# Kernel tuning notes

Hardware: AMD Instinct MI355X
Metric: run time of the kernel (lower is better)

Reference implementation:

```python
import jax, jax.numpy as jnp
import numpy as np

B = 4
NV = 6890           # SMPL vertex count
NF0 = 13776         # SMPL face count (before fill_back)
T = 3               # tex_size
IMG = 128           # render image size
UVH = UVW = 256     # uv image resolution
FLENGTH = 500.0
NEAR, FAR = 0.1, 25.0
CHUNK = 128         # faces per z-buffer scan step
BIG = jnp.float32(1e10)


def setup_inputs():
    key = jax.random.key(0)
    ks = jax.random.split(key, 5)
    faces0 = jax.random.randint(ks[0], (NF0, 3), 0, NV, dtype=jnp.int32)
    faces = jnp.concatenate([faces0, faces0[:, ::-1]], axis=0)  # fill_back
    cam = jnp.concatenate([0.8 + 0.2 * jax.random.uniform(ks[1], (B, 1)),
                           0.05 * jax.random.normal(ks[2], (B, 2))], axis=1)
    vertices = 0.3 * jax.random.normal(ks[3], (B, NV, 3))
    uv_imgs = jax.random.uniform(ks[4], (B, 3, UVH, UVW))
    img2uv_sampler = jax.random.uniform(jax.random.fold_in(key, 7),
                                        (faces.shape[0], T * T, 2)) * 2.0 - 1.0
    return {"cam": cam, "vertices": vertices, "uv_imgs": uv_imgs,
            "img2uv_sampler": img2uv_sampler, "faces": faces}


def _grid_sample(img, grid):
    # img (B,C,H,W), grid (B,N,2) xy in [-1,1]; bilinear, align_corners=False, zeros padding
    Bc, C, H, W = img.shape
    x = (grid[..., 0] + 1.0) * (W * 0.5) - 0.5
    y = (grid[..., 1] + 1.0) * (H * 0.5) - 0.5
    x0f = jnp.floor(x); y0f = jnp.floor(y)
    wx = x - x0f; wy = y - y0f
    x0 = x0f.astype(jnp.int32); y0 = y0f.astype(jnp.int32)
    imgf = img.reshape(Bc, C, H * W)
    def gat(yi, xi, w):
        valid = (xi >= 0) & (xi < W) & (yi >= 0) & (yi < H)
        idx = jnp.clip(yi, 0, H - 1) * W + jnp.clip(xi, 0, W - 1)
        v = jax.vmap(lambda im, i: im[:, i])(imgf, idx)  # (B,C,N)
        return v * (w * valid)[:, None, :]
    return (gat(y0, x0, (1 - wx) * (1 - wy)) + gat(y0, x0 + 1, wx * (1 - wy)) +
            gat(y0 + 1, x0, (1 - wx) * wy) + gat(y0 + 1, x0 + 1, wx * wy))


def _extract_tex(uv_imgs, sampler, nf):
    # sampler (B,nf,T*T,2) -> textures (B,nf,T,T,T,3)
    tex = _grid_sample(uv_imgs, sampler.reshape(uv_imgs.shape[0], -1, 2))
    tex = tex.reshape(-1, 3, nf, T, T).transpose(0, 2, 3, 4, 1)  # (B,nf,T,T,3)
    return jnp.broadcast_to(tex[:, :, :, :, None, :], tex.shape[:4] + (T, 3))


def _lighting(face_verts, textures):
    # module defaults: ambient intensity 1, directional 0, white lights, dir=(0,1,0)
    v0, v1, v2 = face_verts[:, :, 0], face_verts[:, :, 1], face_verts[:, :, 2]
    n = jnp.cross(v1 - v0, v2 - v0)
    n = n / (jnp.linalg.norm(n, axis=-1, keepdims=True) + 1e-10)
    cos = jnp.maximum(n @ jnp.array([0.0, 1.0, 0.0]), 0.0)       # (B,F)
    light = 1.0 * jnp.ones(3) + 0.0 * cos[..., None] * jnp.ones(3)  # (B,F,3)
    return textures * light[:, :, None, None, None, :]


def _weak_projection(cam, vertices):
    p = IMG / 2.0
    tz = FLENGTH / (p * cam[:, 0:1])                              # (B,1)
    v2d = cam[:, None, 0:1] * (vertices[:, :, :2] + cam[:, None, 1:])
    return jnp.concatenate([v2d, vertices[:, :, 2:3] + tz[:, None, :]], axis=-1)


def _bary(fv, px, py):
    # fv: (...,3,3) triangle screen verts; px,py broadcastable pixel coords
    x0 = fv[..., 0, 0]; y0 = fv[..., 0, 1]
    x1 = fv[..., 1, 0]; y1 = fv[..., 1, 1]
    x2 = fv[..., 2, 0]; y2 = fv[..., 2, 1]
    w0 = (x2 - x1) * (py - y1) - (y2 - y1) * (px - x1)
    w1 = (x0 - x2) * (py - y2) - (y0 - y2) * (px - x2)
    w2 = (x1 - x0) * (py - y0) - (y1 - y0) * (px - x0)
    area = w0 + w1 + w2
    s = jnp.where(area == 0, 1.0, area)
    return w0 / s, w1 / s, w2 / s, area


def _pixel_grid():
    xs = (2.0 * jnp.arange(IMG) + 1.0) / IMG - 1.0                # (W,)
    ys = (1.0 - (2.0 * jnp.arange(IMG) + 1.0) / IMG)[:, None]     # (H,1), +y up
    return xs, ys


def _rasterize_fim(face_verts):
    # face_verts (B,F,3,3) in screen coords -> face index map (B,H,W), -1 = bg
    Bc, F = face_verts.shape[:2]
    pad = (-F) % CHUNK
    fv = jnp.pad(face_verts, ((0, 0), (0, pad), (0, 0), (0, 0)))
    S = (F + pad) // CHUNK
    fv = fv.reshape(Bc, S, CHUNK, 3, 3).transpose(1, 0, 2, 3, 4)  # (S,B,C,3,3)
    xs, ys = _pixel_grid()
    def step(carry, inp):
        zbuf, fim = carry
        f, base = inp
        fe = f[:, :, None, None, :, :]                            # (B,C,1,1,3,3)
        b0, b1, b2, area = _bary(fe, xs, ys)                      # (B,C,H,W)
        z0 = f[:, :, 0, 2][..., None, None]
        z1 = f[:, :, 1, 2][..., None, None]
        z2 = f[:, :, 2, 2][..., None, None]
        invz = b0 / z0 + b1 / z1 + b2 / z2                        # perspective-correct
        zp = 1.0 / jnp.where(invz == 0, 1.0, invz)
        inside = (b0 >= 0) & (b1 >= 0) & (b2 >= 0) & (area > 0)   # front-facing only
        valid = inside & (zp > NEAR) & (zp < FAR)
        depth = jnp.where(valid, zp, BIG)
        dmin = jnp.min(depth, axis=1)                             # (B,H,W)
        amin = jnp.argmin(depth, axis=1).astype(jnp.int32) + base
        better = dmin < zbuf
        return (jnp.where(better, dmin, zbuf),
                jnp.where(better, amin, fim)), None
    zbuf0 = jnp.full((Bc, IMG, IMG), BIG)
    fim0 = jnp.full((Bc, IMG, IMG), -1, jnp.int32)
    bases = (jnp.arange(S) * CHUNK).astype(jnp.int32)
    (zbuf, fim), _ = jax.lax.scan(step, (zbuf0, fim0), (fv, bases))
    return fim


def _shade(face_verts, textures, fim):
    # nearest-texel barycentric texture lookup, as in neural_renderer forward
    Bc, F = face_verts.shape[:2]
    fid = jnp.clip(fim, 0, F - 1).reshape(Bc, -1)                 # (B,HW)
    fv = jax.vmap(lambda v, i: v[i])(face_verts, fid)             # (B,HW,3,3)
    fv = fv.reshape(Bc, IMG, IMG, 3, 3)
    xs, ys = _pixel_grid()
    b0, b1, b2, _ = _bary(fv, xs, ys)                             # (B,H,W)
    t0 = jnp.clip(jnp.floor(b0 * T).astype(jnp.int32), 0, T - 1)
    t1 = jnp.clip(jnp.floor(b1 * T).astype(jnp.int32), 0, T - 1)
    t2 = jnp.clip(jnp.floor(b2 * T).astype(jnp.int32), 0, T - 1)
    idx = ((jnp.clip(fim, 0, F - 1) * T + t0) * T + t1) * T + t2  # (B,H,W)
    texf = textures.reshape(Bc, F * T * T * T, 3)
    col = jax.vmap(lambda t, i: t[i])(texf, idx.reshape(Bc, -1))  # (B,HW,3)
    col = col.reshape(Bc, IMG, IMG, 3)
    col = jnp.where((fim >= 0)[..., None], col, 0.0)              # bg color (0,0,0)
    return col.transpose(0, 3, 1, 2)                              # (B,3,H,W)


def reference(cam, vertices, uv_imgs, img2uv_sampler, faces):
    Bc = cam.shape[0]
    nf = faces.shape[0]
    sampler = jnp.broadcast_to(img2uv_sampler[None], (Bc,) + img2uv_sampler.shape)
    textures = _extract_tex(uv_imgs, sampler, nf)                 # (B,nf,T,T,T,3)
    textures = _lighting(vertices[:, faces], textures)
    verts_p = _weak_projection(cam, vertices)
    fv = verts_p[:, faces]                                        # (B,nf,3,3)
    fv_sg = jax.lax.stop_gradient(fv)  # hard rasterization is non-differentiable
    fim = _rasterize_fim(fv_sg)
    images = _shade(fv_sg, textures, fim)
    return images


if __name__ == "__main__":
    out = reference(**setup_inputs())
    print(out.shape, out.dtype)
```

## Files before the change

### kernel.cpp

```cpp
#include <hip/hip_runtime.h>
#include <stdint.h>

#pragma clang fp contract(off)

#define B_    4
#define NV_   6890
#define NF_   27552
#define IMG_  128
#define UV_   256
#define NPIX  (IMG_*IMG_)

#define TS_     8
#define TPB_    (IMG_/TS_)
#define NTILE_  (TPB_*TPB_)
#define NBIN_   (B_*NTILE_)
#define LIST_CAP (2*1024*1024)
#define MAXC_   (LIST_CAP/256 + NBIN_)

__global__ void __launch_bounds__(256) project_k(
    const float* __restrict__ cam, const float* __restrict__ verts,
    float* __restrict__ vp) {
  int idx = blockIdx.x * 256 + threadIdx.x;
  if (idx >= B_ * NV_) return;
  int b = idx / NV_;
  float c0 = cam[b * 3 + 0], c1 = cam[b * 3 + 1], c2 = cam[b * 3 + 2];
  float tz = 500.0f / (64.0f * c0);
  const float* src = verts + (size_t)idx * 3;
  float* dst = vp + (size_t)idx * 3;
  dst[0] = c0 * (src[0] + c1);
  dst[1] = c0 * (src[1] + c2);
  dst[2] = src[2] + tz;
}

__device__ __forceinline__ int face_tiles(
    const float* __restrict__ vp, const int* __restrict__ faces, int b, int f,
    int& tx0, int& tx1, int& ty0, int& ty1, unsigned& z16) {
  int ia = faces[f * 3 + 0], ib = faces[f * 3 + 1], ic = faces[f * 3 + 2];
  const float* vb = vp + (size_t)b * NV_ * 3;
  float x0 = vb[ia * 3 + 0], y0 = vb[ia * 3 + 1];
  float x1 = vb[ib * 3 + 0], y1 = vb[ib * 3 + 1];
  float x2 = vb[ic * 3 + 0], y2 = vb[ic * 3 + 1];
  float area_c = (x1 - x0) * (y2 - y0) - (y1 - y0) * (x2 - x0);
  if (area_c < -1e-3f) return 0;
  float xmn = fminf(x0, fminf(x1, x2)), xmx = fmaxf(x0, fmaxf(x1, x2));
  float ymn = fminf(y0, fminf(y1, y2)), ymx = fmaxf(y0, fmaxf(y1, y2));
  int jlo = (int)floorf((xmn + 1.0f) * 64.0f - 0.5f) - 1;
  int jhi = (int)ceilf ((xmx + 1.0f) * 64.0f - 0.5f) + 1;
  int ilo = (int)floorf((1.0f - ymx) * 64.0f - 0.5f) - 1;
  int ihi = (int)ceilf ((1.0f - ymn) * 64.0f - 0.5f) + 1;
  if (jhi < 0 || ihi < 0 || jlo > IMG_ - 1 || ilo > IMG_ - 1) return 0;
  jlo = max(jlo, 0); ilo = max(ilo, 0);
  jhi = min(jhi, IMG_ - 1); ihi = min(ihi, IMG_ - 1);
  tx0 = jlo >> 3; tx1 = jhi >> 3; ty0 = ilo >> 3; ty1 = ihi >> 3;
  float z0 = vb[ia * 3 + 2], z1 = vb[ib * 3 + 2], z2 = vb[ic * 3 + 2];
  z16 = __float_as_uint(fminf(z0, fminf(z1, z2))) >> 16;
  return 1;
}

__global__ void __launch_bounds__(256) bin_count_k(
    const float* __restrict__ vp, const int* __restrict__ faces,
    int* __restrict__ cnt, int* __restrict__ rects) {
  __shared__ int scnt[NTILE_];
  int f = blockIdx.x * 256 + threadIdx.x;
  int b = blockIdx.y;
  scnt[threadIdx.x] = 0;
  __syncthreads();
  int tx0, tx1, ty0, ty1;
  unsigned z16 = 0;
  int valid =
      (f < NF_) ? face_tiles(vp, faces, b, f, tx0, tx1, ty0, ty1, z16) : 0;
  if (f < NF_)
    rects[(size_t)b * NF_ + f] =
        valid ? (int)((z16 << 16) | (unsigned)(tx0 | (tx1 << 4) | (ty0 << 8) |
                                               (ty1 << 12)))
              : (int)0xFFFF0000u;
  if (valid)
    for (int ty = ty0; ty <= ty1; ++ty)
      for (int tx = tx0; tx <= tx1; ++tx)
        atomicAdd(&scnt[ty * TPB_ + tx], 1);
  __syncthreads();
  int t = threadIdx.x;
  int v = scnt[t];
  if (v > 0) atomicAdd(&cnt[b * NTILE_ + t], v);
}

__global__ void __launch_bounds__(1024) scan_k(
    const int* __restrict__ cnt, int* __restrict__ off, int* __restrict__ cur,
    int* __restrict__ work, int* __restrict__ nC) {
  __shared__ int sm[NBIN_];
  int t = threadIdx.x;
  int v = cnt[t];
  sm[t] = v;
  __syncthreads();
  for (int d = 1; d < NBIN_; d <<= 1) {
    int u = (t >= d) ? sm[t - d] : 0;
    __syncthreads();
    sm[t] += u;
    __syncthreads();
  }
  int o = sm[t] - v;
  off[t] = o;
  cur[t] = o;
  int nch = (max(v - 256, 0) + 255) >> 8;
  __syncthreads();
  sm[t] = nch;
  __syncthreads();
  for (int d = 1; d < NBIN_; d <<= 1) {
    int u = (t >= d) ? sm[t - d] : 0;
    __syncthreads();
    sm[t] += u;
    __syncthreads();
  }
  int cb = sm[t] - nch;
  if (t == NBIN_ - 1) nC[0] = sm[t];
  for (int c = 0; c < nch; ++c) work[cb + c] = t | ((c + 1) << 10);
}

__global__ void __launch_bounds__(256) bin_fill_k(
    const int* __restrict__ rects, int* __restrict__ cur,
    int* __restrict__ list) {
  __shared__ int scnt[NTILE_];
  __shared__ int sbase[NTILE_];
  int f = blockIdx.x * 256 + threadIdx.x;
  int b = blockIdx.y;
  scnt[threadIdx.x] = 0;
  __syncthreads();
  unsigned rv =
      (f < NF_) ? (unsigned)rects[(size_t)b * NF_ + f] : 0xFFFF0000u;
  unsigned hi = rv >> 16;
  int valid = (hi != 0xFFFFu);
  int tx0 = rv & 15, tx1 = (rv >> 4) & 15;
  int ty0 = (rv >> 8) & 15, ty1 = (rv >> 12) & 15;
  if (valid)
    for (int ty = ty0; ty <= ty1; ++ty)
      for (int tx = tx0; tx <= tx1; ++tx)
        atomicAdd(&scnt[ty * TPB_ + tx], 1);
  __syncthreads();
  int t = threadIdx.x;
  int v = scnt[t];
  if (v > 0) sbase[t] = atomicAdd(&cur[b * NTILE_ + t], v);
  __syncthreads();
  scnt[t] = 0;
  __syncthreads();
  if (valid) {
    int ev = (int)((hi << 15) | (unsigned)f);
    for (int ty = ty0; ty <= ty1; ++ty)
      for (int tx = tx0; tx <= tx1; ++tx) {
        int bin = ty * TPB_ + tx;
        int r = atomicAdd(&scnt[bin], 1);
        int slot = sbase[bin] + r;
        if (slot < LIST_CAP) list[slot] = ev;
      }
  }
}

__device__ __forceinline__ void raster_slice(
    const float4 (*F)[64], int nsurv, float px, float py,
    unsigned long long& kb, unsigned& kbz_u) {
  unsigned win_u = 0x7F800000u;
  unsigned long long qm = 0ull;
  for (int q = 0; q < nsurv; ++q) {
    float4 A = F[0][q];
    float4 Bv = F[1][q];
    float4 Cv = F[2][q];
    float w0 = A.x * (py - A.w) - A.y * (px - A.z);
    float w1 = Bv.x * (py - Bv.w) - Bv.y * (px - Bv.z);
    float w2 = Cv.x * (py - Cv.w) - Cv.y * (px - Cv.z);
    float area = (w0 + w1) + w2;
    float mn = fminf(w0, fminf(w1, w2));
    bool pred = (area > 0.0f) && !(mn < 0.0f);
    if (!__any(pred)) continue;
    float4 P = F[4][q];
    float num = (w0 * P.x + w1 * P.y) + w2 * P.z;
    float zpa = (area * P.w) * __builtin_amdgcn_rcpf(num);
    unsigned cu = win_u < kbz_u ? win_u : kbz_u;
    float thrq = __uint_as_float(cu) * 1.001f;
    bool amb = pred && (!(zpa > thrq) ||
                        (zpa > 0.09989f && zpa < 0.10011f) ||
                        (zpa > 24.9724f && zpa < 25.0276f));
    if (amb) qm |= 1ull << q;
    bool ok = pred && (zpa > 0.1001f) && (zpa < 24.975f);
    unsigned zb = __float_as_uint(zpa);
    if (ok && zb < win_u) win_u = zb;
  }
  while (__any(qm != 0ull)) {
    if (qm != 0ull) {
      int q = __ffsll(qm) - 1;
      qm &= qm - 1ull;
      float4 A = F[0][q];
      float4 Bv = F[1][q];
      float4 Cv = F[2][q];
      float w0 = A.x * (py - A.w) - A.y * (px - A.z);
      float w1 = Bv.x * (py - Bv.w) - Bv.y * (px - Bv.z);
      float w2 = Cv.x * (py - Cv.w) - Cv.y * (px - Cv.z);
      float area = (w0 + w1) + w2;
      float4 P = F[4][q];
      float num = (w0 * P.x + w1 * P.y) + w2 * P.z;
      float zpa = (area * P.w) * __builtin_amdgcn_rcpf(num);
      unsigned cu = win_u < kbz_u ? win_u : kbz_u;
      float thrf = __uint_as_float(cu) * 1.001f;
      if (!(zpa > thrf) ||
          (zpa > 0.09989f && zpa < 0.10011f) ||
          (zpa > 24.9724f && zpa < 25.0276f)) {
        float4 Z = F[3][q];
        float b0 = w0 / area, b1 = w1 / area, b2 = w2 / area;
        float invz = (b0 / Z.x + b1 / Z.y) + b2 / Z.z;
        float zp = 1.0f / (invz == 0.0f ? 1.0f : invz);
        if (zp > 0.1f && zp < 25.0f) {
          unsigned long long key =
              ((unsigned long long)__float_as_uint(zp) << 32) |
              (unsigned int)__float_as_int(Z.w);
          if (key < kb) {
            kb = key;
            kbz_u = (unsigned)(kb >> 32);
          }
        }
      }
    }
  }
}

__device__ __forceinline__ void stage_face(
    float4 (*F)[64], const float* __restrict__ vb,
    const int* __restrict__ faces, int fid, int rank) {
  int ia = faces[fid * 3 + 0], ib = faces[fid * 3 + 1], ic = faces[fid * 3 + 2];
  float X0 = vb[ia * 3 + 0], Y0 = vb[ia * 3 + 1], Z0 = vb[ia * 3 + 2];
  float X1 = vb[ib * 3 + 0], Y1 = vb[ib * 3 + 1], Z1 = vb[ib * 3 + 2];
  float X2 = vb[ic * 3 + 0], Y2 = vb[ic * 3 + 1], Z2 = vb[ic * 3 + 2];
  F[0][rank] = make_float4(X2 - X1, Y2 - Y1, X1, Y1);
  F[1][rank] = make_float4(X0 - X2, Y0 - Y2, X2, Y2);
  F[2][rank] = make_float4(X1 - X0, Y1 - Y0, X0, Y0);
  F[3][rank] = make_float4(Z0, Z1, Z2, __int_as_float(fid));
  F[4][rank] = make_float4(Z1 * Z2, Z0 * Z2, Z0 * Z1, Z0 * Z1 * Z2);
}

__global__ void __launch_bounds__(256) raster_seed_k(
    const float* __restrict__ vp, const int* __restrict__ faces,
    const int* __restrict__ list, const int* __restrict__ cnt,
    const int* __restrict__ off, unsigned long long* __restrict__ zkey) {
  __shared__ float4 fd[4][5][64];
  __shared__ unsigned long long mg[4][64];
  int bin = blockIdx.x;
  int b = bin >> 8;
  int t = bin & 255;
  int tyT = t >> 4, txT = t & 15;
  int ws = threadIdx.x >> 6, lane = threadIdx.x & 63;
  int pi = tyT * TS_ + (lane >> 3);
  int pj = txT * TS_ + (lane & 7);
  float px = fmaf((float)pj, 0.015625f, -0.9921875f);
  float py = fmaf((float)pi, -0.015625f, 0.9921875f);

  int n = min(cnt[bin], 256);
  int base = off[bin];
  int seg = ws * 64;
  int mw = min(n - seg, 64);

  unsigned long long kb = ~0ull;
  unsigned kbz_u = 0x7F800000u;
  if (mw > 0) {
    if (lane < mw) {
      int fid = (int)((unsigned)list[base + seg + lane] & 0x7FFFu);
      stage_face(fd[ws], vp + (size_t)b * NV_ * 3, faces, fid, lane);
    }
    raster_slice(fd[ws], mw, px, py, kb, kbz_u);
  }

  mg[ws][lane] = kb;
  __syncthreads();
  if (ws == 0) {
    unsigned long long k0 = mg[0][lane];
    unsigned long long k1 = mg[1][lane];
    unsigned long long k2 = mg[2][lane];
    unsigned long long k3 = mg[3][lane];
    k0 = k1 < k0 ? k1 : k0;
    k2 = k3 < k2 ? k3 : k2;
    k0 = k2 < k0 ? k2 : k0;
    zkey[(size_t)b * NPIX + pi * IMG_ + pj] = k0;
  }
}

__global__ void __launch_bounds__(256) raster_k(
    const float* __restrict__ vp, const int* __restrict__ faces,
    const int* __restrict__ list, const int* __restrict__ cnt,
    const int* __restrict__ off, const int* __restrict__ work,
    const int* __restrict__ nC, unsigned long long* __restrict__ zkey) {
  __shared__ float4 fd[4][5][64];
  __shared__ unsigned long long mg[4][64];
  __shared__ unsigned sdz[64];
  int bid = blockIdx.x;
  if (bid >= nC[0]) return;
  int wkv = work[bid];
  int bin = wkv & (NBIN_ - 1);
  int chunk = wkv >> 10;
  int b = bin >> 8;
  int t = bin & 255;
  int tyT = t >> 4, txT = t & 15;
  int ws = threadIdx.x >> 6, lane = threadIdx.x & 63;
  int pi = tyT * TS_ + (lane >> 3);
  int pj = txT * TS_ + (lane & 7);
  float px = fmaf((float)pj, 0.015625f, -0.9921875f);
  float py = fmaf((float)pi, -0.015625f, 0.9921875f);

  if (threadIdx.x < 64) {
    unsigned long long s = atomicMin(
        zkey + (size_t)b * NPIX + (tyT * TS_ + (threadIdx.x >> 3)) * IMG_ +
            txT * TS_ + (threadIdx.x & 7),
        ~0ull);
    sdz[threadIdx.x] = (unsigned)(s >> 32);
  }
  __syncthreads();

  unsigned seed_u = min(sdz[lane], 0x7F800000u);
  unsigned mx = seed_u;
  for (int j = 1; j < 64; j <<= 1) {
    unsigned o = (unsigned)__shfl_xor((int)mx, j, 64);
    mx = o > mx ? o : mx;
  }
  unsigned thr_code = __float_as_uint(__uint_as_float(mx) * 1.01f) >> 16;

  int n = cnt[bin];
  int seg = (chunk << 8) + (ws << 6);
  int base0 = off[bin] + seg;
  int mw = min(n - seg, 64);
  mw = max(mw, 0);

  bool live = false;
  int fid = 0;
  if (lane < mw) {
    unsigned e = (unsigned)list[base0 + lane];
    live = ((e >> 15) <= thr_code);
    fid = (int)(e & 0x7FFFu);
  }
  unsigned long long bal = __ballot(live);
  unsigned long long kb = ~0ull;
  unsigned kbz_u = seed_u;
  if (bal != 0ull) {
    int nsurv = (int)__popcll(bal);
    int rank = (int)__popcll(bal & ((1ull << lane) - 1ull));
    if (live)
      stage_face(fd[ws], vp + (size_t)b * NV_ * 3, faces, fid, rank);
    raster_slice(fd[ws], nsurv, px, py, kb, kbz_u);
  }

  mg[ws][lane] = kb;
  __syncthreads();
  if (ws == 0) {
    unsigned long long k0 = mg[0][lane];
    unsigned long long k1 = mg[1][lane];
    unsigned long long k2 = mg[2][lane];
    unsigned long long k3 = mg[3][lane];
    k0 = k1 < k0 ? k1 : k0;
    k2 = k3 < k2 ? k3 : k2;
    k0 = k2 < k0 ? k2 : k0;
    if (k0 != ~0ull)
      atomicMin(zkey + (size_t)b * NPIX + pi * IMG_ + pj, k0);
  }
}

#define TAP(ty, tx, wexpr)                                                   \
  {                                                                          \
    int ty_ = (ty), tx_ = (tx);                                              \
    float w_ = (wexpr);                                                      \
    float valid_ =                                                           \
        (tx_ >= 0 && tx_ < UV_ && ty_ >= 0 && ty_ < UV_) ? 1.0f : 0.0f;      \
    float wv_ = w_ * valid_;                                                 \
    int cy_ = min(max(ty_, 0), UV_ - 1), cx_ = min(max(tx_, 0), UV_ - 1);    \
    int o_ = cy_ * UV_ + cx_;                                                \
    cr = cr + img[o_] * wv_;                                                 \
    cg = cg + img[UV_ * UV_ + o_] * wv_;                                     \
    cb = cb + img[2 * UV_ * UV_ + o_] * wv_;                                 \
  }

__global__ void __launch_bounds__(256) shade_k(
    const float* __restrict__ vp, const int* __restrict__ faces,
    const float* __restrict__ uv, const float* __restrict__ samp,
    const unsigned long long* __restrict__ zkey, float* __restrict__ out) {
  int idx = blockIdx.x * 256 + threadIdx.x;
  if (idx >= B_ * NPIX) return;
  int b = idx / NPIX;
  int p = idx - b * NPIX;
  int ii = p / IMG_;
  int jj = p - ii * IMG_;

  unsigned long long key = zkey[idx];
  float cr = 0.0f, cg = 0.0f, cb = 0.0f;
  if (key != 0xFFFFFFFFFFFFFFFFull) {
    int f = (int)(key & 0xFFFFFFFFull);
    int ia = faces[f * 3 + 0], ib = faces[f * 3 + 1], ic = faces[f * 3 + 2];
    const float* vb = vp + (size_t)b * NV_ * 3;
    float x0 = vb[ia * 3 + 0], y0 = vb[ia * 3 + 1];
    float x1 = vb[ib * 3 + 0], y1 = vb[ib * 3 + 1];
    float x2 = vb[ic * 3 + 0], y2 = vb[ic * 3 + 1];
    float px = (float)(2 * jj + 1) / 128.0f - 1.0f;
    float py = 1.0f - (float)(2 * ii + 1) / 128.0f;
    float w0 = (x2 - x1) * (py - y1) - (y2 - y1) * (px - x1);
    float w1 = (x0 - x2) * (py - y2) - (y0 - y2) * (px - x2);
    float w2 = (x1 - x0) * (py - y0) - (y1 - y0) * (px - x0);
    float area = (w0 + w1) + w2;
    float s = (area == 0.0f) ? 1.0f : area;
    float b0 = w0 / s, b1 = w1 / s;
    int t0 = min(max((int)floorf(b0 * 3.0f), 0), 2);
    int t1 = min(max((int)floorf(b1 * 3.0f), 0), 2);

    const float* g = samp + ((size_t)f * 9 + (size_t)(t0 * 3 + t1)) * 2;
    float gx = g[0], gy = g[1];
    float x = (gx + 1.0f) * 128.0f - 0.5f;
    float y = (gy + 1.0f) * 128.0f - 0.5f;
    float x0f = floorf(x), y0f = floorf(y);
    float wx = x - x0f, wy = y - y0f;
    int xi = (int)x0f, yi = (int)y0f;
    float omwx = 1.0f - wx, omwy = 1.0f - wy;
    const float* img = uv + (size_t)b * 3 * UV_ * UV_;
    TAP(yi,     xi,     omwx * omwy)
    TAP(yi,     xi + 1, wx * omwy)
    TAP(yi + 1, xi,     omwx * wy)
    TAP(yi + 1, xi + 1, wx * wy)
  }
  out[((size_t)b * 3 + 0) * NPIX + p] = cr;
  out[((size_t)b * 3 + 1) * NPIX + p] = cg;
  out[((size_t)b * 3 + 2) * NPIX + p] = cb;
}

extern "C" void kernel_launch(void* const* d_in, const int* in_sizes, int n_in,
                              void* d_out, int out_size, void* d_ws,
                              size_t ws_size, hipStream_t stream) {
  const float* cam   = (const float*)d_in[0];
  const float* verts = (const float*)d_in[1];
  const float* uv    = (const float*)d_in[2];
  const float* samp  = (const float*)d_in[3];
  const int*   faces = (const int*)d_in[4];

  char* ws = (char*)d_ws;
  size_t o = 0;
  unsigned long long* zkey = (unsigned long long*)(ws + o);
  o += (size_t)B_ * NPIX * 8;
  float* vp = (float*)(ws + o);
  o += ((size_t)B_ * NV_ * 3 * 4 + 1023) & ~1023ull;
  int* cnt   = (int*)(ws + o); o += NBIN_ * 4;
  int* offs  = (int*)(ws + o); o += NBIN_ * 4;
  int* cur   = (int*)(ws + o); o += NBIN_ * 4;
  int* nC    = (int*)(ws + o); o += 1024;
  int* work  = (int*)(ws + o); o += (size_t)MAXC_ * 4;
  int* rects = (int*)(ws + o); o += (size_t)B_ * NF_ * 4;
  int* list  = (int*)(ws + o);

  hipMemsetAsync(cnt, 0, NBIN_ * 4, stream);
  project_k<<<(B_ * NV_ + 255) / 256, 256, 0, stream>>>(cam, verts, vp);
  dim3 bgrid((NF_ + 255) / 256, B_);
  bin_count_k<<<bgrid, 256, 0, stream>>>(vp, faces, cnt, rects);
  scan_k<<<1, NBIN_, 0, stream>>>(cnt, offs, cur, work, nC);
  bin_fill_k<<<bgrid, 256, 0, stream>>>(rects, cur, list);
  raster_seed_k<<<NBIN_, 256, 0, stream>>>(vp, faces, list, cnt, offs, zkey);
  raster_k<<<MAXC_, 256, 0, stream>>>(vp, faces, list, cnt, offs, work, nC,
                                      zkey);
  shade_k<<<(B_ * NPIX + 255) / 256, 256, 0, stream>>>(vp, faces, uv, samp,
                                                       zkey, (float*)d_out);
}
```

Baseline: 182.4 us.

## Add exact triangle-tile culling and depth-bucketed bin lists for raster

Binning now rejects tiles that a triangle's edge functions fully exclude, and sorts each tile's face list into 8 coarse depth buckets so nearer faces come first. Lists are split into a float z array and a 16-bit face-id array, and the raster threshold compares exact zmin against a tighter bound. Vertices are padded to float4 for vector loads, and the scan uses wave shuffles. The aim is fewer face-pixel tests and better early depth culling in raster_k. The cost is recomputing face binning in bin_fill instead of reusing rects, and depth buckets tuned to hard-coded z thresholds.

```diff
diff --git a/kernel.cpp b/kernel.cpp
--- a/kernel.cpp
+++ b/kernel.cpp
@@ -14,7 +14,9 @@
 #define TPB_    (IMG_/TS_)
 #define NTILE_  (TPB_*TPB_)
 #define NBIN_   (B_*NTILE_)
-#define LIST_CAP (2*1024*1024)
+#define NZ_     8
+#define NCELL_  (NTILE_*NZ_)
+#define LIST_CAP (1536*1024)
 #define MAXC_   (LIST_CAP/256 + NBIN_)
 
 __global__ void __launch_bounds__(256) project_k(
@@ -26,132 +28,177 @@
   float c0 = cam[b * 3 + 0], c1 = cam[b * 3 + 1], c2 = cam[b * 3 + 2];
   float tz = 500.0f / (64.0f * c0);
   const float* src = verts + (size_t)idx * 3;
-  float* dst = vp + (size_t)idx * 3;
+  float* dst = vp + (size_t)idx * 4;
   dst[0] = c0 * (src[0] + c1);
   dst[1] = c0 * (src[1] + c2);
   dst[2] = src[2] + tz;
-}
-
-__device__ __forceinline__ int face_tiles(
-    const float* __restrict__ vp, const int* __restrict__ faces, int b, int f,
-    int& tx0, int& tx1, int& ty0, int& ty1, unsigned& z16) {
+  dst[3] = 0.0f;
+}
+
+struct FaceBin {
+  int valid, tx0, tx1, ty0, ty1, bu;
+  float d21x, d21y, d02x, d02y, d10x, d10y;
+  float x0, y0, x1, y1, x2, y2, zmin;
+};
+
+__device__ __forceinline__ FaceBin face_bin(
+    const float* __restrict__ cam, const float* __restrict__ vp,
+    const int* __restrict__ faces, int b, int f) {
+  FaceBin r; r.valid = 0;
   int ia = faces[f * 3 + 0], ib = faces[f * 3 + 1], ic = faces[f * 3 + 2];
-  const float* vb = vp + (size_t)b * NV_ * 3;
-  float x0 = vb[ia * 3 + 0], y0 = vb[ia * 3 + 1];
-  float x1 = vb[ib * 3 + 0], y1 = vb[ib * 3 + 1];
-  float x2 = vb[ic * 3 + 0], y2 = vb[ic * 3 + 1];
+  const float* vb = vp + (size_t)b * NV_ * 4;
+  float x0 = vb[ia * 4 + 0], y0 = vb[ia * 4 + 1], z0 = vb[ia * 4 + 2];
+  float x1 = vb[ib * 4 + 0], y1 = vb[ib * 4 + 1], z1 = vb[ib * 4 + 2];
+  float x2 = vb[ic * 4 + 0], y2 = vb[ic * 4 + 1], z2 = vb[ic * 4 + 2];
   float area_c = (x1 - x0) * (y2 - y0) - (y1 - y0) * (x2 - x0);
-  if (area_c < -1e-3f) return 0;
+  if (area_c < -1e-3f) return r;
   float xmn = fminf(x0, fminf(x1, x2)), xmx = fmaxf(x0, fmaxf(x1, x2));
   float ymn = fminf(y0, fminf(y1, y2)), ymx = fmaxf(y0, fmaxf(y1, y2));
   int jlo = (int)floorf((xmn + 1.0f) * 64.0f - 0.5f) - 1;
   int jhi = (int)ceilf ((xmx + 1.0f) * 64.0f - 0.5f) + 1;
   int ilo = (int)floorf((1.0f - ymx) * 64.0f - 0.5f) - 1;
   int ihi = (int)ceilf ((1.0f - ymn) * 64.0f - 0.5f) + 1;
-  if (jhi < 0 || ihi < 0 || jlo > IMG_ - 1 || ilo > IMG_ - 1) return 0;
+  if (jhi < 0 || ihi < 0 || jlo > IMG_ - 1 || ilo > IMG_ - 1) return r;
   jlo = max(jlo, 0); ilo = max(ilo, 0);
   jhi = min(jhi, IMG_ - 1); ihi = min(ihi, IMG_ - 1);
-  tx0 = jlo >> 3; tx1 = jhi >> 3; ty0 = ilo >> 3; ty1 = ihi >> 3;
-  float z0 = vb[ia * 3 + 2], z1 = vb[ib * 3 + 2], z2 = vb[ic * 3 + 2];
-  z16 = __float_as_uint(fminf(z0, fminf(z1, z2))) >> 16;
-  return 1;
+  r.tx0 = jlo >> 3; r.tx1 = jhi >> 3; r.ty0 = ilo >> 3; r.ty1 = ihi >> 3;
+  r.zmin = fminf(z0, fminf(z1, z2));
+  float tz = 500.0f / (64.0f * cam[b * 3]);
+  float zr = r.zmin - tz;
+  r.bu = (zr > -0.447f) + (zr > -0.367f) + (zr > -0.308f) + (zr > -0.254f) +
+         (zr > -0.200f) + (zr > -0.141f) + (zr > -0.061f);
+  r.d21x = x2 - x1; r.d21y = y2 - y1;
+  r.d02x = x0 - x2; r.d02y = y0 - y2;
+  r.d10x = x1 - x0; r.d10y = y1 - y0;
+  r.x0 = x0; r.y0 = y0; r.x1 = x1; r.y1 = y1; r.x2 = x2; r.y2 = y2;
+  r.valid = 1;
+  return r;
+}
+
+__device__ __forceinline__ int tile_pass(const FaceBin& r, int tx, int ty) {
+  float pxmin = fmaf((float)(tx * 8), 0.015625f, -0.9921875f);
+  float pxmax = pxmin + 0.109375f;
+  float pymax = fmaf((float)(ty * 8), -0.015625f, 0.9921875f);
+  float pymin = pymax - 0.109375f;
+  float w0m = r.d21x * ((r.d21x > 0.0f ? pymax : pymin) - r.y1) -
+              r.d21y * ((r.d21y > 0.0f ? pxmin : pxmax) - r.x1);
+  float w1m = r.d02x * ((r.d02x > 0.0f ? pymax : pymin) - r.y2) -
+              r.d02y * ((r.d02y > 0.0f ? pxmin : pxmax) - r.x2);
+  float w2m = r.d10x * ((r.d10x > 0.0f ? pymax : pymin) - r.y0) -
+              r.d10y * ((r.d10y > 0.0f ? pxmin : pxmax) - r.x0);
+  return (w0m >= -1e-3f) && (w1m >= -1e-3f) && (w2m >= -1e-3f);
 }
 
 __global__ void __launch_bounds__(256) bin_count_k(
-    const float* __restrict__ vp, const int* __restrict__ faces,
-    int* __restrict__ cnt, int* __restrict__ rects) {
-  __shared__ int scnt[NTILE_];
+    const float* __restrict__ cam, const float* __restrict__ vp,
+    const int* __restrict__ faces, int* __restrict__ cnt8) {
+  __shared__ int scnt[NCELL_];
   int f = blockIdx.x * 256 + threadIdx.x;
   int b = blockIdx.y;
-  scnt[threadIdx.x] = 0;
-  __syncthreads();
-  int tx0, tx1, ty0, ty1;
-  unsigned z16 = 0;
-  int valid =
-      (f < NF_) ? face_tiles(vp, faces, b, f, tx0, tx1, ty0, ty1, z16) : 0;
-  if (f < NF_)
-    rects[(size_t)b * NF_ + f] =
-        valid ? (int)((z16 << 16) | (unsigned)(tx0 | (tx1 << 4) | (ty0 << 8) |
-                                               (ty1 << 12)))
-              : (int)0xFFFF0000u;
-  if (valid)
-    for (int ty = ty0; ty <= ty1; ++ty)
-      for (int tx = tx0; tx <= tx1; ++tx)
-        atomicAdd(&scnt[ty * TPB_ + tx], 1);
-  __syncthreads();
+  for (int k = threadIdx.x; k < NCELL_; k += 256) scnt[k] = 0;
+  __syncthreads();
+  if (f < NF_) {
+    FaceBin r = face_bin(cam, vp, faces, b, f);
+    if (r.valid)
+      for (int ty = r.ty0; ty <= r.ty1; ++ty)
+        for (int tx = r.tx0; tx <= r.tx1; ++tx)
+          if (tile_pass(r, tx, ty))
+            atomicAdd(&scnt[(ty * TPB_ + tx) * NZ_ + r.bu], 1);
+  }
+  __syncthreads();
+  for (int k = threadIdx.x; k < NCELL_; k += 256) {
+    int v = scnt[k];
+    if (v > 0) atomicAdd(&cnt8[(size_t)b * NCELL_ + k], v);
+  }
+}
+
+__global__ void __launch_bounds__(1024) scan_k(
+    const int* __restrict__ cnt8, int* __restrict__ off8,
+    int* __restrict__ cur8, int* __restrict__ binoff,
+    int* __restrict__ bintot, int* __restrict__ work, int* __restrict__ nC) {
+  __shared__ int wsum[16];
   int t = threadIdx.x;
-  int v = scnt[t];
-  if (v > 0) atomicAdd(&cnt[b * NTILE_ + t], v);
-}
-
-__global__ void __launch_bounds__(1024) scan_k(
-    const int* __restrict__ cnt, int* __restrict__ off, int* __restrict__ cur,
-    int* __restrict__ work, int* __restrict__ nC) {
-  __shared__ int sm[NBIN_];
-  int t = threadIdx.x;
-  int v = cnt[t];
-  sm[t] = v;
-  __syncthreads();
-  for (int d = 1; d < NBIN_; d <<= 1) {
-    int u = (t >= d) ? sm[t - d] : 0;
-    __syncthreads();
-    sm[t] += u;
-    __syncthreads();
-  }
-  int o = sm[t] - v;
-  off[t] = o;
-  cur[t] = o;
-  int nch = (max(v - 256, 0) + 255) >> 8;
-  __syncthreads();
-  sm[t] = nch;
-  __syncthreads();
-  for (int d = 1; d < NBIN_; d <<= 1) {
-    int u = (t >= d) ? sm[t - d] : 0;
-    __syncthreads();
-    sm[t] += u;
-    __syncthreads();
-  }
-  int cb = sm[t] - nch;
-  if (t == NBIN_ - 1) nC[0] = sm[t];
-  for (int c = 0; c < nch; ++c) work[cb + c] = t | ((c + 1) << 10);
+  int lane = t & 63, w = t >> 6;
+  int c[NZ_];
+  int s = 0;
+#pragma unroll
+  for (int j = 0; j < NZ_; ++j) { c[j] = cnt8[t * NZ_ + j]; s += c[j]; }
+  int inc = s;
+#pragma unroll
+  for (int d = 1; d < 64; d <<= 1) {
+    int u = __shfl_up(inc, d, 64);
+    if (lane >= d) inc += u;
+  }
+  if (lane == 63) wsum[w] = inc;
+  __syncthreads();
+  int wb = 0;
+  for (int k = 0; k < 16; ++k) wb += (k < w) ? wsum[k] : 0;
+  int base = wb + inc - s;
+  int o = base;
+#pragma unroll
+  for (int j = 0; j < NZ_; ++j) {
+    off8[t * NZ_ + j] = o;
+    cur8[t * NZ_ + j] = o;
+    o += c[j];
+  }
+  binoff[t] = base;
+  bintot[t] = s;
+  int nch = (max(s - 256, 0) + 255) >> 8;
+  int inc2 = nch;
+#pragma unroll
+  for (int d = 1; d < 64; d <<= 1) {
+    int u = __shfl_up(inc2, d, 64);
+    if (lane >= d) inc2 += u;
+  }
+  __syncthreads();
+  if (lane == 63) wsum[w] = inc2;
+  __syncthreads();
+  int wb2 = 0;
+  for (int k = 0; k < 16; ++k) wb2 += (k < w) ? wsum[k] : 0;
+  int cb = wb2 + inc2 - nch;
+  if (t == 1023) nC[0] = wb2 + inc2;
+  for (int q = 0; q < nch; ++q) work[cb + q] = t | ((q + 1) << 10);
 }
 
 __global__ void __launch_bounds__(256) bin_fill_k(
-    const int* __restrict__ rects, int* __restrict__ cur,
-    int* __restrict__ list) {
-  __shared__ int scnt[NTILE_];
-  __shared__ int sbase[NTILE_];
+    const float* __restrict__ cam, const float* __restrict__ vp,
+    const int* __restrict__ faces, int* __restrict__ cur8,
+    float* __restrict__ zarr, unsigned short* __restrict__ fidarr) {
+  __shared__ int scnt[NCELL_];
+  __shared__ int sbase[NCELL_];
   int f = blockIdx.x * 256 + threadIdx.x;
   int b = blockIdx.y;
-  scnt[threadIdx.x] = 0;
-  __syncthreads();
-  unsigned rv =
-      (f < NF_) ? (unsigned)rects[(size_t)b * NF_ + f] : 0xFFFF0000u;
-  unsigned hi = rv >> 16;
-  int valid = (hi != 0xFFFFu);
-  int tx0 = rv & 15, tx1 = (rv >> 4) & 15;
-  int ty0 = (rv >> 8) & 15, ty1 = (rv >> 12) & 15;
-  if (valid)
-    for (int ty = ty0; ty <= ty1; ++ty)
-      for (int tx = tx0; tx <= tx1; ++tx)
-        atomicAdd(&scnt[ty * TPB_ + tx], 1);
-  __syncthreads();
-  int t = threadIdx.x;
-  int v = scnt[t];
-  if (v > 0) sbase[t] = atomicAdd(&cur[b * NTILE_ + t], v);
-  __syncthreads();
-  scnt[t] = 0;
-  __syncthreads();
-  if (valid) {
-    int ev = (int)((hi << 15) | (unsigned)f);
-    for (int ty = ty0; ty <= ty1; ++ty)
-      for (int tx = tx0; tx <= tx1; ++tx) {
-        int bin = ty * TPB_ + tx;
-        int r = atomicAdd(&scnt[bin], 1);
-        int slot = sbase[bin] + r;
-        if (slot < LIST_CAP) list[slot] = ev;
-      }
-  }
+  for (int k = threadIdx.x; k < NCELL_; k += 256) scnt[k] = 0;
+  __syncthreads();
+  FaceBin r; r.valid = 0;
+  if (f < NF_) {
+    r = face_bin(cam, vp, faces, b, f);
+    if (r.valid)
+      for (int ty = r.ty0; ty <= r.ty1; ++ty)
+        for (int tx = r.tx0; tx <= r.tx1; ++tx)
+          if (tile_pass(r, tx, ty))
+            atomicAdd(&scnt[(ty * TPB_ + tx) * NZ_ + r.bu], 1);
+  }
+  __syncthreads();
+  for (int k = threadIdx.x; k < NCELL_; k += 256) {
+    int v = scnt[k];
+    if (v > 0) sbase[k] = atomicAdd(&cur8[(size_t)b * NCELL_ + k], v);
+  }
+  __syncthreads();
+  for (int k = threadIdx.x; k < NCELL_; k += 256) scnt[k] = 0;
+  __syncthreads();
+  if (r.valid)
+    for (int ty = r.ty0; ty <= r.ty1; ++ty)
+      for (int tx = r.tx0; tx <= r.tx1; ++tx)
+        if (tile_pass(r, tx, ty)) {
+          int cell = (ty * TPB_ + tx) * NZ_ + r.bu;
+          int rk = atomicAdd(&scnt[cell], 1);
+          int slot = sbase[cell] + rk;
+          if (slot < LIST_CAP) {
+            zarr[slot] = r.zmin;
+            fidarr[slot] = (unsigned short)f;
+          }
+        }
 }
 
 __device__ __forceinline__ void raster_slice(
@@ -224,20 +271,22 @@
     float4 (*F)[64], const float* __restrict__ vb,
     const int* __restrict__ faces, int fid, int rank) {
   int ia = faces[fid * 3 + 0], ib = faces[fid * 3 + 1], ic = faces[fid * 3 + 2];
-  float X0 = vb[ia * 3 + 0], Y0 = vb[ia * 3 + 1], Z0 = vb[ia * 3 + 2];
-  float X1 = vb[ib * 3 + 0], Y1 = vb[ib * 3 + 1], Z1 = vb[ib * 3 + 2];
-  float X2 = vb[ic * 3 + 0], Y2 = vb[ic * 3 + 1], Z2 = vb[ic * 3 + 2];
-  F[0][rank] = make_float4(X2 - X1, Y2 - Y1, X1, Y1);
-  F[1][rank] = make_float4(X0 - X2, Y0 - Y2, X2, Y2);
-  F[2][rank] = make_float4(X1 - X0, Y1 - Y0, X0, Y0);
-  F[3][rank] = make_float4(Z0, Z1, Z2, __int_as_float(fid));
-  F[4][rank] = make_float4(Z1 * Z2, Z0 * Z2, Z0 * Z1, Z0 * Z1 * Z2);
+  float4 v0 = *(const float4*)(vb + (size_t)ia * 4);
+  float4 v1 = *(const float4*)(vb + (size_t)ib * 4);
+  float4 v2 = *(const float4*)(vb + (size_t)ic * 4);
+  F[0][rank] = make_float4(v2.x - v1.x, v2.y - v1.y, v1.x, v1.y);
+  F[1][rank] = make_float4(v0.x - v2.x, v0.y - v2.y, v2.x, v2.y);
+  F[2][rank] = make_float4(v1.x - v0.x, v1.y - v0.y, v0.x, v0.y);
+  F[3][rank] = make_float4(v0.z, v1.z, v2.z, __int_as_float(fid));
+  F[4][rank] =
+      make_float4(v1.z * v2.z, v0.z * v2.z, v0.z * v1.z, v0.z * v1.z * v2.z);
 }
 
 __global__ void __launch_bounds__(256) raster_seed_k(
     const float* __restrict__ vp, const int* __restrict__ faces,
-    const int* __restrict__ list, const int* __restrict__ cnt,
-    const int* __restrict__ off, unsigned long long* __restrict__ zkey) {
+    const unsigned short* __restrict__ fidarr,
+    const int* __restrict__ bintot, const int* __restrict__ binoff,
+    unsigned long long* __restrict__ zkey) {
   __shared__ float4 fd[4][5][64];
   __shared__ unsigned long long mg[4][64];
   int bin = blockIdx.x;
@@ -250,8 +299,8 @@
   float px = fmaf((float)pj, 0.015625f, -0.9921875f);
   float py = fmaf((float)pi, -0.015625f, 0.9921875f);
 
-  int n = min(cnt[bin], 256);
-  int base = off[bin];
+  int n = min(bintot[bin], 256);
+  int base = binoff[bin];
   int seg = ws * 64;
   int mw = min(n - seg, 64);
 
@@ -259,8 +308,8 @@
   unsigned kbz_u = 0x7F800000u;
   if (mw > 0) {
     if (lane < mw) {
-      int fid = (int)((unsigned)list[base + seg + lane] & 0x7FFFu);
-      stage_face(fd[ws], vp + (size_t)b * NV_ * 3, faces, fid, lane);
+      int fid = (int)fidarr[base + seg + lane];
+      stage_face(fd[ws], vp + (size_t)b * NV_ * 4, faces, fid, lane);
     }
     raster_slice(fd[ws], mw, px, py, kb, kbz_u);
   }
@@ -281,12 +330,12 @@
 
 __global__ void __launch_bounds__(256) raster_k(
     const float* __restrict__ vp, const int* __restrict__ faces,
-    const int* __restrict__ list, const int* __restrict__ cnt,
-    const int* __restrict__ off, const int* __restrict__ work,
-    const int* __restrict__ nC, unsigned long long* __restrict__ zkey) {
+    const float* __restrict__ zarr, const unsigned short* __restrict__ fidarr,
+    const int* __restrict__ bintot, const int* __restrict__ binoff,
+    const int* __restrict__ work, const int* __restrict__ nC,
+    unsigned long long* __restrict__ zkey) {
   __shared__ float4 fd[4][5][64];
   __shared__ unsigned long long mg[4][64];
-  __shared__ unsigned sdz[64];
   int bid = blockIdx.x;
   if (bid >= nC[0]) return;
   int wkv = work[bid];
@@ -301,44 +350,34 @@
   float px = fmaf((float)pj, 0.015625f, -0.9921875f);
   float py = fmaf((float)pi, -0.015625f, 0.9921875f);
 
-  if (threadIdx.x < 64) {
-    unsigned long long s = atomicMin(
-        zkey + (size_t)b * NPIX + (tyT * TS_ + (threadIdx.x >> 3)) * IMG_ +
-            txT * TS_ + (threadIdx.x & 7),
-        ~0ull);
-    sdz[threadIdx.x] = (unsigned)(s >> 32);
-  }
-  __syncthreads();
-
-  unsigned seed_u = min(sdz[lane], 0x7F800000u);
+  const unsigned* zhi = (const unsigned*)zkey;
+  unsigned seed_u =
+      min(zhi[((size_t)b * NPIX + pi * IMG_ + pj) * 2 + 1], 0x7F800000u);
   unsigned mx = seed_u;
   for (int j = 1; j < 64; j <<= 1) {
     unsigned o = (unsigned)__shfl_xor((int)mx, j, 64);
     mx = o > mx ? o : mx;
   }
-  unsigned thr_code = __float_as_uint(__uint_as_float(mx) * 1.01f) >> 16;
-
-  int n = cnt[bin];
+  float thrf = __uint_as_float(mx) * 1.001f;
+
+  int n = bintot[bin];
   int seg = (chunk << 8) + (ws << 6);
-  int base0 = off[bin] + seg;
+  int base0 = binoff[bin] + seg;
   int mw = min(n - seg, 64);
   mw = max(mw, 0);
 
   bool live = false;
-  int fid = 0;
-  if (lane < mw) {
-    unsigned e = (unsigned)list[base0 + lane];
-    live = ((e >> 15) <= thr_code);
-    fid = (int)(e & 0x7FFFu);
-  }
+  if (lane < mw) live = (zarr[base0 + lane] <= thrf);
   unsigned long long bal = __ballot(live);
   unsigned long long kb = ~0ull;
   unsigned kbz_u = seed_u;
   if (bal != 0ull) {
     int nsurv = (int)__popcll(bal);
     int rank = (int)__popcll(bal & ((1ull << lane) - 1ull));
-    if (live)
-      stage_face(fd[ws], vp + (size_t)b * NV_ * 3, faces, fid, rank);
+    if (live) {
+      int fid = (int)fidarr[base0 + lane];
+      stage_face(fd[ws], vp + (size_t)b * NV_ * 4, faces, fid, rank);
+    }
     raster_slice(fd[ws], nsurv, px, py, kb, kbz_u);
   }
 
@@ -387,10 +426,10 @@
   if (key != 0xFFFFFFFFFFFFFFFFull) {
     int f = (int)(key & 0xFFFFFFFFull);
     int ia = faces[f * 3 + 0], ib = faces[f * 3 + 1], ic = faces[f * 3 + 2];
-    const float* vb = vp + (size_t)b * NV_ * 3;
-    float x0 = vb[ia * 3 + 0], y0 = vb[ia * 3 + 1];
-    float x1 = vb[ib * 3 + 0], y1 = vb[ib * 3 + 1];
-    float x2 = vb[ic * 3 + 0], y2 = vb[ic * 3 + 1];
+    const float* vb = vp + (size_t)b * NV_ * 4;
+    float x0 = vb[ia * 4 + 0], y0 = vb[ia * 4 + 1];
+    float x1 = vb[ib * 4 + 0], y1 = vb[ib * 4 + 1];
+    float x2 = vb[ic * 4 + 0], y2 = vb[ic * 4 + 1];
     float px = (float)(2 * jj + 1) / 128.0f - 1.0f;
     float py = 1.0f - (float)(2 * ii + 1) / 128.0f;
     float w0 = (x2 - x1) * (py - y1) - (y2 - y1) * (px - x1);
@@ -435,24 +474,27 @@
   unsigned long long* zkey = (unsigned long long*)(ws + o);
   o += (size_t)B_ * NPIX * 8;
   float* vp = (float*)(ws + o);
-  o += ((size_t)B_ * NV_ * 3 * 4 + 1023) & ~1023ull;
-  int* cnt   = (int*)(ws + o); o += NBIN_ * 4;
-  int* offs  = (int*)(ws + o); o += NBIN_ * 4;
-  int* cur   = (int*)(ws + o); o += NBIN_ * 4;
-  int* nC    = (int*)(ws + o); o += 1024;
-  int* work  = (int*)(ws + o); o += (size_t)MAXC_ * 4;
-  int* rects = (int*)(ws + o); o += (size_t)B_ * NF_ * 4;
-  int* list  = (int*)(ws + o);
-
-  hipMemsetAsync(cnt, 0, NBIN_ * 4, stream);
+  o += ((size_t)B_ * NV_ * 4 * 4 + 1023) & ~1023ull;
+  int* cnt8   = (int*)(ws + o); o += (size_t)NBIN_ * NZ_ * 4;
+  int* off8   = (int*)(ws + o); o += (size_t)NBIN_ * NZ_ * 4;
+  int* cur8   = (int*)(ws + o); o += (size_t)NBIN_ * NZ_ * 4;
+  int* binoff = (int*)(ws + o); o += NBIN_ * 4;
+  int* bintot = (int*)(ws + o); o += NBIN_ * 4;
+  int* nC     = (int*)(ws + o); o += 1024;
+  int* work   = (int*)(ws + o); o += (size_t)MAXC_ * 4;
+  float* zarr = (float*)(ws + o); o += (size_t)LIST_CAP * 4;
+  unsigned short* fidarr = (unsigned short*)(ws + o);
+
+  hipMemsetAsync(cnt8, 0, (size_t)NBIN_ * NZ_ * 4, stream);
   project_k<<<(B_ * NV_ + 255) / 256, 256, 0, stream>>>(cam, verts, vp);
   dim3 bgrid((NF_ + 255) / 256, B_);
-  bin_count_k<<<bgrid, 256, 0, stream>>>(vp, faces, cnt, rects);
-  scan_k<<<1, NBIN_, 0, stream>>>(cnt, offs, cur, work, nC);
-  bin_fill_k<<<bgrid, 256, 0, stream>>>(rects, cur, list);
-  raster_seed_k<<<NBIN_, 256, 0, stream>>>(vp, faces, list, cnt, offs, zkey);
-  raster_k<<<MAXC_, 256, 0, stream>>>(vp, faces, list, cnt, offs, work, nC,
-                                      zkey);
+  bin_count_k<<<bgrid, 256, 0, stream>>>(cam, vp, faces, cnt8);
+  scan_k<<<1, NBIN_, 0, stream>>>(cnt8, off8, cur8, binoff, bintot, work, nC);
+  bin_fill_k<<<bgrid, 256, 0, stream>>>(cam, vp, faces, cur8, zarr, fidarr);
+  raster_seed_k<<<NBIN_, 256, 0, stream>>>(vp, faces, fidarr, bintot, binoff,
+                                           zkey);
+  raster_k<<<MAXC_, 256, 0, stream>>>(vp, faces, zarr, fidarr, bintot, binoff,
+                                      work, nC, zkey);
   shade_k<<<(B_ * NPIX + 255) / 256, 256, 0, stream>>>(vp, faces, uv, samp,
                                                        zkey, (float*)d_out);
 }
```

Measured after the change: 191.3 us. +4.9%, slower.
